# Kernel optimization log

Measured on AMD Instinct MI355X. Metric: run time of the kernel, lower is better.

Reference implementation:

```python
import jax, jax.numpy as jnp
import numpy as np

B = 1024
N_ATOMS = 51
FLAT = 7 * 7 * 64  # conv output: 84->20->9->7 spatial, 64 channels


def _conv(x, w, b, s):
    # x: NCHW, w: OIHW, VALID padding, stride s
    y = jax.lax.conv_general_dilated(
        x, w, window_strides=(s, s), padding='VALID',
        dimension_numbers=('NCHW', 'OIHW', 'NCHW'))
    return y + b[None, :, None, None]


def setup_inputs() -> dict:
    key = jax.random.key(0)
    ks = jax.random.split(key, 8)

    def w(k, shape, fan_in):
        return jax.random.normal(k, shape, dtype=jnp.float32) / np.float32(np.sqrt(fan_in))

    return {
        'x': jax.random.uniform(ks[0], (B, 4, 84, 84), jnp.float32, 0.0, 256.0),
        'cw1': w(ks[1], (32, 4, 8, 8), 4 * 8 * 8), 'cb1': jnp.zeros((32,), jnp.float32),
        'cw2': w(ks[2], (64, 32, 4, 4), 32 * 4 * 4), 'cb2': jnp.zeros((64,), jnp.float32),
        'cw3': w(ks[3], (64, 64, 3, 3), 64 * 3 * 3), 'cb3': jnp.zeros((64,), jnp.float32),
        'fw1': w(ks[4], (FLAT, 256), FLAT), 'fb1': jnp.zeros((256,), jnp.float32),
        'fw2': w(ks[5], (256, N_ATOMS), 256), 'fb2': jnp.zeros((N_ATOMS,), jnp.float32),
        'z': jnp.linspace(-10.0, 10.0, N_ATOMS).astype(jnp.float32),  # support atoms
        'n_out': 6,
    }


def reference(x, cw1, cb1, cw2, cb2, cw3, cb3, fw1, fb1, fw2, fb2, z, n_out):
    x = x / 256.0
    x = jax.nn.relu(_conv(x, cw1, cb1, 4))  # [B,32,20,20]
    x = jax.nn.relu(_conv(x, cw2, cb2, 2))  # [B,64,9,9]
    x = jax.nn.relu(_conv(x, cw3, cb3, 1))  # [B,64,7,7]
    h = x.reshape(x.shape[0], -1)           # [B,3136]
    h = jax.nn.relu(h @ fw1 + fb1)          # [B,256]
    p = jax.nn.softmax(h @ fw2 + fb2, axis=1)  # [B,n_atoms]
    # Original loop writes fc_layers(x)[i] identically for every action j:
    dist = jnp.broadcast_to(p[:, None, :], (p.shape[0], n_out, p.shape[1]))
    res = jnp.einsum('bna,a->bn', dist, z)  # expected value per action
    return (dist, res)
```

## Files before the change

kernel.cpp:

```cpp
#include <hip/hip_runtime.h>
#include <hip/hip_fp16.h>

#define RL(x) __builtin_amdgcn_readfirstlane(x)

typedef _Float16 f16x8 __attribute__((ext_vector_type(8)));
typedef float    f32x16 __attribute__((ext_vector_type(16)));

__global__ __launch_bounds__(256) void wprep_k(const float* __restrict__ w1,
                                               const float* __restrict__ w2,
                                               const float* __restrict__ w3,
                                               __half* __restrict__ w1h,
                                               __half* __restrict__ w2h,
                                               float* __restrict__ wt3) {
  int i = blockIdx.x * 256 + threadIdx.x;
  if (i < 8192) {
    int kx = i & 7, oc = (i >> 3) & 31, ky = (i >> 8) & 7, ic = i >> 11;
    w1h[i] = __float2half(w1[oc * 256 + ic * 64 + ky * 8 + kx] * 0.00390625f);
  }
  if (i < 32768) {
    int j = i & 7, ln = (i >> 3) & 31, kh = (i >> 8) & 1, ot = (i >> 9) & 1, ic = i >> 10;
    int k = kh * 8 + j, kx = k >> 2, ky = k & 3, oc = ot * 32 + ln;
    w2h[i] = __float2half(w2[oc * 512 + ic * 16 + ky * 4 + kx]);
  }
  if (i < 36864) {
    int o3 = i % 24, o = o3 / 3, kx = o3 - o * 3;
    int r = i / 24, ocg = r & 7, r2 = r >> 3, ky = r2 % 3, ic = r2 / 3;
    wt3[i] = w3[(ocg * 8 + o) * 576 + ic * 9 + ky * 3 + kx];
  }
}

__global__ __launch_bounds__(256, 2) void conv1_k(const float* __restrict__ x,
                                                  const __half* __restrict__ w1h,
                                                  const float* __restrict__ bias,
                                                  __half* __restrict__ out) {
  const int b = blockIdx.x;
  const int tid = threadIdx.x;
  const int lane = tid & 63;
  const int wv   = RL(tid >> 6);
  const int kh = lane >> 5;
  const int ln = lane & 31;
  const int nt = (wv == 0) ? 4 : 3;

  int ibs[4], pvv[4];
#pragma unroll
  for (int tt = 0; tt < 4; ++tt) {
    int p = (wv + tt * 4) * 32 + ln;
    pvv[tt] = (p < 400);
    if (p > 399) p = 399;
    int py = p / 20, px = p - py * 20;
    ibs[tt] = py * 336 + px * 4;
  }

  f32x16 acc[4];
#pragma unroll
  for (int tt = 0; tt < 4; ++tt)
#pragma unroll
    for (int r = 0; r < 16; ++r) acc[tt][r] = 0.f;

  const float* xb = x + b * 28224;

#pragma unroll 1
  for (int ic = 0; ic < 4; ++ic) {
#pragma unroll
    for (int t = 0; t < 4; ++t) {
      f16x8 aw = *(const f16x8*)(w1h + ((ic * 8 + 2 * t + kh) * 32 + ln) * 8);
      const float* rp = xb + ic * 7056 + (2 * t + kh) * 84;
#pragma unroll
      for (int tt = 0; tt < 4; ++tt) {
        if (tt < nt) {
          const float* ap = rp + ibs[tt];
          float4 lo = *(const float4*)ap;
          float4 hi = *(const float4*)(ap + 4);
          __half2 p0 = __floats2half2_rn(lo.x, lo.y);
          __half2 p1 = __floats2half2_rn(lo.z, lo.w);
          __half2 p2 = __floats2half2_rn(hi.x, hi.y);
          __half2 p3 = __floats2half2_rn(hi.z, hi.w);
          uint4 u = make_uint4(*(unsigned*)&p0, *(unsigned*)&p1,
                               *(unsigned*)&p2, *(unsigned*)&p3);
          f16x8 bx = *(f16x8*)&u;
          acc[tt] = __builtin_amdgcn_mfma_f32_32x32x16_f16(aw, bx, acc[tt], 0, 0, 0);
        }
      }
    }
  }

  float bv[16];
#pragma unroll
  for (int r = 0; r < 16; ++r)
    bv[r] = bias[(r & 3) + 8 * (r >> 2) + 4 * kh];

#pragma unroll
  for (int tt = 0; tt < 4; ++tt) {
    if (tt < nt && pvv[tt]) {
      const int p = (wv + tt * 4) * 32 + ln;
#pragma unroll
      for (int r = 0; r < 16; ++r) {
        const int oc = (r & 3) + 8 * (r >> 2) + 4 * kh;
        float v = acc[tt][r] + bv[r];
        out[b * 12800 + oc * 400 + p] = __float2half(v > 0.f ? v : 0.f);
      }
    }
  }
}

__global__ __launch_bounds__(256) void t1_k(const __half* __restrict__ in,
                                            __half* __restrict__ out) {
  __shared__ __half t[64][65];
  const int kb = blockIdx.x * 64;
  const int bb = blockIdx.y * 64;
  const int lane = threadIdx.x & 63;
  const int ty   = threadIdx.x >> 6;
#pragma unroll
  for (int r = ty; r < 64; r += 4)
    t[r][lane] = in[(bb + r) * 12800 + kb + lane];
  __syncthreads();
#pragma unroll
  for (int r = ty; r < 64; r += 4)
    out[(kb + r) * 1024 + bb + lane] = t[lane][r];
}

__global__ __launch_bounds__(256, 1) void conv2_k(const __half* __restrict__ in,
                                                  const __half* __restrict__ w2h,
                                                  const float* __restrict__ bias,
                                                  __half* __restrict__ out) {
  __shared__ __align__(16) __half sh[2][9216];
  const int bid = blockIdx.x;
  const int opy = bid % 9;
  const int bt  = bid / 9;
  const int bbase = bt * 64;
  const int tid  = threadIdx.x;
  const int lane = tid & 63;
  const int wv   = RL(tid >> 6);
  const int octile = wv & 1;
  const int bsub   = wv >> 1;
  const int kh = lane >> 5;
  const int ln = lane & 31;

  const unsigned short* inu = (const unsigned short*)in;
  const unsigned short* wu  = (const unsigned short*)w2h;

  int roff[5], offA[5];
#pragma unroll
  for (int p = 0; p < 5; ++p) {
    int idx = p * 256 + tid;
    int px = idx >> 6, b = idx & 63;
    roff[p] = px * 1024 + b;
    offA[p] = b * 128 + ((((px >> 1) ^ (b & 7)) << 3) | ((px & 1) << 2));
  }
  const int base0 = (40 * opy) * 1024 + bbase;

  f32x16 acc[9];
#pragma unroll
  for (int ox = 0; ox < 9; ++ox)
#pragma unroll
    for (int r = 0; r < 16; ++r) acc[ox][r] = 0.f;

  ushort4 s0, s1, s2, s3, s4; uint2 sW;

#define C2_LOAD(icv) do {                                                     \
    const unsigned short* ibp = inu + (icv) * 409600 + base0;                 \
    s0 = make_ushort4(ibp[roff[0]], ibp[roff[0]+20480], ibp[roff[0]+40960], ibp[roff[0]+61440]); \
    s1 = make_ushort4(ibp[roff[1]], ibp[roff[1]+20480], ibp[roff[1]+40960], ibp[roff[1]+61440]); \
    s2 = make_ushort4(ibp[roff[2]], ibp[roff[2]+20480], ibp[roff[2]+40960], ibp[roff[2]+61440]); \
    s3 = make_ushort4(ibp[roff[3]], ibp[roff[3]+20480], ibp[roff[3]+40960], ibp[roff[3]+61440]); \
    s4 = make_ushort4(ibp[roff[4]], ibp[roff[4]+20480], ibp[roff[4]+40960], ibp[roff[4]+61440]); \
    sW = *(const uint2*)(wu + (icv) * 1024 + tid * 4);                        \
  } while (0)

#define C2_STORE(buf) do {                                                    \
    *(uint2*)&sh[buf][offA[0]] = make_uint2((unsigned)s0.x | ((unsigned)s0.y << 16), (unsigned)s0.z | ((unsigned)s0.w << 16)); \
    *(uint2*)&sh[buf][offA[1]] = make_uint2((unsigned)s1.x | ((unsigned)s1.y << 16), (unsigned)s1.z | ((unsigned)s1.w << 16)); \
    *(uint2*)&sh[buf][offA[2]] = make_uint2((unsigned)s2.x | ((unsigned)s2.y << 16), (unsigned)s2.z | ((unsigned)s2.w << 16)); \
    *(uint2*)&sh[buf][offA[3]] = make_uint2((unsigned)s3.x | ((unsigned)s3.y << 16), (unsigned)s3.z | ((unsigned)s3.w << 16)); \
    *(uint2*)&sh[buf][offA[4]] = make_uint2((unsigned)s4.x | ((unsigned)s4.y << 16), (unsigned)s4.z | ((unsigned)s4.w << 16)); \
    *(uint2*)&sh[buf][8192 + tid * 4] = sW;                                   \
  } while (0)

  const int offW = 8192 + octile * 512 + kh * 256 + ln * 8;
  const int bloc = bsub * 32 + ln;
  const int bx7  = bloc & 7;
  const int brow = bloc * 128;

  int cur = 0;
  C2_LOAD(0);
#pragma unroll 1
  for (int ic = 0; ic < 32; ++ic) {
    __syncthreads();
    C2_STORE(cur);
    const int icn = ic < 31 ? ic + 1 : 31;
    C2_LOAD(icn);
    __syncthreads();
    f16x8 aw = *(const f16x8*)&sh[cur][offW];
#pragma unroll
    for (int ox = 0; ox < 9; ++ox) {
      f16x8 bx = *(const f16x8*)&sh[cur][brow + (((ox + kh) ^ bx7) << 3)];
      acc[ox] = __builtin_amdgcn_mfma_f32_32x32x16_f16(aw, bx, acc[ox], 0, 0, 0);
    }
    cur ^= 1;
  }
#undef C2_LOAD
#undef C2_STORE

  float bv[16];
#pragma unroll
  for (int r = 0; r < 16; ++r)
    bv[r] = bias[octile * 32 + (r & 3) + 8 * (r >> 2) + 4 * kh];
  const int bout = bbase + bloc;
#pragma unroll
  for (int ox = 0; ox < 9; ++ox) {
#pragma unroll
    for (int r = 0; r < 16; ++r) {
      const int oc = octile * 32 + (r & 3) + 8 * (r >> 2) + 4 * kh;
      float v = acc[ox][r] + bv[r];
      out[(oc * 81 + opy * 9 + ox) * 1024 + bout] = __float2half(v > 0.f ? v : 0.f);
    }
  }
}

__global__ __launch_bounds__(128, 2) void conv3_k(const __half* __restrict__ in,
                                                  const float* __restrict__ wt,
                                                  const float* __restrict__ bias,
                                                  __half* __restrict__ out) {
  const int bid = blockIdx.x;
  const int ocg = (bid >> 3) & 15;
  const int grp = ((bid >> 7) << 3) | (bid & 7);
  const int opy = grp % 7;
  const int bg  = grp / 7;
  const int tid  = threadIdx.x;
  const int lane = tid & 63;
  const int wv   = RL(tid >> 6);

  float acc[4][7];
#pragma unroll
  for (int o = 0; o < 4; ++o)
#pragma unroll
    for (int ox = 0; ox < 7; ++ox) acc[o][ox] = 0.f;

  const __half* ib = in + bg * 64 + lane;
  const int ic0 = wv * 32;

#pragma unroll 1
  for (int ici = 0; ici < 32; ++ici) {
    const int ic = ic0 + ici;
#pragma unroll
    for (int ky = 0; ky < 3; ++ky) {
      const float* wp = wt + ((ic * 3 + ky) * 8 + (ocg >> 1)) * 24 + (ocg & 1) * 12;
      float wk[12];
#pragma unroll
      for (int q = 0; q < 12; ++q) wk[q] = wp[q];
      const __half* rp = ib + (ic * 81 + (opy + ky) * 9) * 1024;
      float iv[9];
#pragma unroll
      for (int q = 0; q < 9; ++q) iv[q] = __half2float(rp[q * 1024]);
#pragma unroll
      for (int o = 0; o < 4; ++o)
#pragma unroll
        for (int ox = 0; ox < 7; ++ox)
#pragma unroll
          for (int kx = 0; kx < 3; ++kx)
            acc[o][ox] = fmaf(iv[ox + kx], wk[o * 3 + kx], acc[o][ox]);
    }
  }

  __shared__ float red[4][7][64];
  if (wv == 1) {
#pragma unroll
    for (int o = 0; o < 4; ++o)
#pragma unroll
      for (int ox = 0; ox < 7; ++ox) red[o][ox][lane] = acc[o][ox];
  }
  __syncthreads();
  if (wv == 0) {
#pragma unroll
    for (int o = 0; o < 4; ++o) {
      const int oc = ocg * 4 + o;
      const float bj = bias[oc];
#pragma unroll
      for (int ox = 0; ox < 7; ++ox) {
        float v = acc[o][ox] + red[o][ox][lane] + bj;
        out[(oc * 49 + opy * 7 + ox) * 1024 + bg * 64 + lane] =
            __float2half(v > 0.f ? v : 0.f);
      }
    }
  }
}

__global__ __launch_bounds__(64, 2) void fc1a_k(const __half* __restrict__ a,
                                                const float* __restrict__ w,
                                                float* __restrict__ part) {
  const int bid = blockIdx.x;
  const int jg  = (bid >> 3) & 15;
  const int grp = ((bid >> 7) << 3) | (bid & 7);
  const int kc  = grp & 15;
  const int bg  = grp >> 4;
  const int lane = threadIdx.x;

  float acc[16];
#pragma unroll
  for (int j = 0; j < 16; ++j) acc[j] = 0.f;

  const __half* ap = a + kc * 196 * 1024 + bg * 64 + lane;
  const float* wp0 = w + kc * 196 * 256 + jg * 16;

#pragma unroll 4
  for (int k = 0; k < 196; ++k) {
    float av = __half2float(ap[k * 1024]);
    const float* wp = wp0 + k * 256;
#pragma unroll
    for (int j = 0; j < 16; ++j) acc[j] = fmaf(av, wp[j], acc[j]);
  }
#pragma unroll
  for (int j = 0; j < 16; ++j)
    part[(kc * 256 + jg * 16 + j) * 1024 + bg * 64 + lane] = acc[j];
}

__global__ __launch_bounds__(256) void fc1b_k(const float* __restrict__ part,
                                              const float* __restrict__ bias,
                                              float* __restrict__ h) {
  int idx = blockIdx.x * 256 + threadIdx.x;
  float s = bias[idx >> 10];
#pragma unroll
  for (int c = 0; c < 16; ++c) s += part[c * 262144 + idx];
  h[idx] = s > 0.f ? s : 0.f;
}

__global__ __launch_bounds__(256) void fc2_k(const float* __restrict__ h,
                                             const float* __restrict__ w,
                                             const float* __restrict__ bias,
                                             const float* __restrict__ z,
                                             float* __restrict__ dist,
                                             float* __restrict__ res) {
  __shared__ float wl[256 * 51];
  const int tid = threadIdx.x;
#pragma unroll
  for (int i = tid; i < 256 * 51; i += 256) wl[i] = w[i];
  __syncthreads();

  const int j   = tid & 63;
  const int b   = blockIdx.x * 4 + RL(tid >> 6);
  const int jc = j < 51 ? j : 50;
  float acc = bias[jc];
#pragma unroll 8
  for (int k = 0; k < 256; ++k)
    acc = fmaf(h[k * 1024 + b], wl[k * 51 + jc], acc);
  float logit = (j < 51) ? acc : -1e30f;
  float m = logit;
#pragma unroll
  for (int o = 32; o > 0; o >>= 1) m = fmaxf(m, __shfl_xor(m, o, 64));
  float e = (j < 51) ? __expf(logit - m) : 0.f;
  float ssum = e;
#pragma unroll
  for (int o = 32; o > 0; o >>= 1) ssum += __shfl_xor(ssum, o, 64);
  float p = e / ssum;
  float zv = (j < 51) ? z[jc] : 0.f;
  float rz = p * zv;
#pragma unroll
  for (int o = 32; o > 0; o >>= 1) rz += __shfl_xor(rz, o, 64);
  if (j < 51) {
    float* db = dist + b * 6 * 51 + j;
#pragma unroll
    for (int n = 0; n < 6; ++n) db[n * 51] = p;
  }
  if (j < 6) res[b * 6 + j] = rz;
}

extern "C" void kernel_launch(void* const* d_in, const int* in_sizes, int n_in,
                              void* d_out, int out_size, void* d_ws, size_t ws_size,
                              hipStream_t stream) {
  const float* x   = (const float*)d_in[0];
  const float* cw1 = (const float*)d_in[1];
  const float* cb1 = (const float*)d_in[2];
  const float* cw2 = (const float*)d_in[3];
  const float* cb2 = (const float*)d_in[4];
  const float* cw3 = (const float*)d_in[5];
  const float* cb3 = (const float*)d_in[6];
  const float* fw1 = (const float*)d_in[7];
  const float* fb1 = (const float*)d_in[8];
  const float* fw2 = (const float*)d_in[9];
  const float* fb2 = (const float*)d_in[10];
  const float* z   = (const float*)d_in[11];

  float* ws = (float*)d_ws;
  __half* c1h = (__half*)ws;
  __half* c1t = (__half*)(ws + 6553600);
  __half* c2t = (__half*)(ws + 13107200);
  __half* c3t = (__half*)(ws + 15761408);
  float*  pw  = ws;
  float*  h_t = ws + 4194304;

  float*  wt3n = (float*)d_out;
  __half* w1h  = (__half*)((float*)d_out + 36864);
  __half* w2h  = (__half*)((float*)d_out + 45056);

  float* dist = (float*)d_out;
  float* res  = dist + 1024 * 6 * 51;

  wprep_k<<<144, 256, 0, stream>>>(cw1, cw2, cw3, w1h, w2h, wt3n);
  conv1_k<<<1024, 256, 0, stream>>>(x, w1h, cb1, c1h);
  t1_k<<<dim3(200, 16), 256, 0, stream>>>(c1h, c1t);
  conv2_k<<<144, 256, 0, stream>>>(c1t, w2h, cb2, c2t);
  conv3_k<<<1792, 128, 0, stream>>>(c2t, wt3n, cb3, c3t);
  fc1a_k<<<4096, 64, 0, stream>>>(c3t, fw1, pw);
  fc1b_k<<<1024, 256, 0, stream>>>(pw, fb1, h_t);
  fc2_k<<<256, 256, 0, stream>>>(h_t, fw2, fb2, z, dist, res);
}
```

Baseline: 395.4 us.

## Rewrite conv3 as f16 MFMA with double-buffered LDS staging

```diff
diff --git a/kernel.cpp b/kernel.cpp
--- a/kernel.cpp
+++ b/kernel.cpp
@@ -4,6 +4,7 @@
 #define RL(x) __builtin_amdgcn_readfirstlane(x)
 
 typedef _Float16 f16x8 __attribute__((ext_vector_type(8)));
+typedef _Float16 f16x4 __attribute__((ext_vector_type(4)));
 typedef float    f32x16 __attribute__((ext_vector_type(16)));
 
 __global__ __launch_bounds__(256) void wprep_k(const float* __restrict__ w1,
@@ -11,7 +12,7 @@
                                                const float* __restrict__ w3,
                                                __half* __restrict__ w1h,
                                                __half* __restrict__ w2h,
-                                               float* __restrict__ wt3) {
+                                               __half* __restrict__ w3h) {
   int i = blockIdx.x * 256 + threadIdx.x;
   if (i < 8192) {
     int kx = i & 7, oc = (i >> 3) & 31, ky = (i >> 8) & 7, ic = i >> 11;
@@ -22,10 +23,11 @@
     int k = kh * 8 + j, kx = k >> 2, ky = k & 3, oc = ot * 32 + ln;
     w2h[i] = __float2half(w2[oc * 512 + ic * 16 + ky * 4 + kx]);
   }
-  if (i < 36864) {
-    int o3 = i % 24, o = o3 / 3, kx = o3 - o * 3;
-    int r = i / 24, ocg = r & 7, r2 = r >> 3, ky = r2 % 3, ic = r2 / 3;
-    wt3[i] = w3[(ocg * 8 + o) * 576 + ic * 9 + ky * 3 + kx];
+  if (i < 65536) {
+    int j = i & 7, ln = (i >> 3) & 31, kh = (i >> 8) & 1, ot = (i >> 9) & 1, ic = i >> 10;
+    int k = kh * 8 + j, kx = k >> 2, ky = k & 3, oc = ot * 32 + ln;
+    float v = (kx < 3 && ky < 3) ? w3[oc * 576 + ic * 9 + ky * 3 + kx] : 0.f;
+    w3h[i] = __float2half(v);
   }
 }
 
@@ -217,70 +219,111 @@
   }
 }
 
-__global__ __launch_bounds__(128, 2) void conv3_k(const __half* __restrict__ in,
-                                                  const float* __restrict__ wt,
+__global__ __launch_bounds__(256, 1) void conv3_k(const __half* __restrict__ in,
+                                                  const __half* __restrict__ w3h,
                                                   const float* __restrict__ bias,
                                                   __half* __restrict__ out) {
+  __shared__ __align__(16) __half sh[2][3840];
   const int bid = blockIdx.x;
-  const int ocg = (bid >> 3) & 15;
-  const int grp = ((bid >> 7) << 3) | (bid & 7);
-  const int opy = grp % 7;
-  const int bg  = grp / 7;
+  const int opy = bid % 7;
+  const int bt  = bid / 7;
+  const int bbase = bt * 64;
   const int tid  = threadIdx.x;
   const int lane = tid & 63;
   const int wv   = RL(tid >> 6);
-
-  float acc[4][7];
-#pragma unroll
-  for (int o = 0; o < 4; ++o)
-#pragma unroll
-    for (int ox = 0; ox < 7; ++ox) acc[o][ox] = 0.f;
-
-  const __half* ib = in + bg * 64 + lane;
-  const int ic0 = wv * 32;
-
+  const int octile = wv & 1;
+  const int bsub   = wv >> 1;
+  const int kh = lane >> 5;
+  const int ln = lane & 31;
+
+  const unsigned short* inu = (const unsigned short*)in;
+  const unsigned short* wu  = (const unsigned short*)w3h;
+
+  int rof[4];
+#pragma unroll
+  for (int ky = 0; ky < 4; ++ky) {
+    int r = opy + ky; if (r > 8) r = 8;
+    rof[ky] = r * 9 * 1024;
+  }
+  int gof[3], sof[3];
+#pragma unroll
+  for (int p = 0; p < 3; ++p) {
+    int idx = p * 256 + tid;
+    int b = idx & 63, px = idx >> 6;
+    int pxc = px > 8 ? 8 : px;
+    gof[p] = pxc * 1024 + bbase + b;
+    sof[p] = b * 44 + px * 4;
+  }
+
+  f32x16 acc[7];
+#pragma unroll
+  for (int ox = 0; ox < 7; ++ox)
+#pragma unroll
+    for (int r = 0; r < 16; ++r) acc[ox][r] = 0.f;
+
+  ushort4 s0, s1, s2; uint2 sW;
+
+#define C3_LOAD(icv) do {                                                     \
+    const unsigned short* ibp = inu + (icv) * 82944;                          \
+    s0 = make_ushort4(ibp[rof[0]+gof[0]], ibp[rof[1]+gof[0]],                 \
+                      ibp[rof[2]+gof[0]], ibp[rof[3]+gof[0]]);                \
+    s1 = make_ushort4(ibp[rof[0]+gof[1]], ibp[rof[1]+gof[1]],                 \
+                      ibp[rof[2]+gof[1]], ibp[rof[3]+gof[1]]);                \
+    if (tid < 128)                                                            \
+      s2 = make_ushort4(ibp[rof[0]+gof[2]], ibp[rof[1]+gof[2]],               \
+                        ibp[rof[2]+gof[2]], ibp[rof[3]+gof[2]]);              \
+    sW = *(const uint2*)(wu + (icv) * 1024 + tid * 4);                        \
+  } while (0)
+
+#define C3_STORE(buf) do {                                                    \
+    *(uint2*)&sh[buf][sof[0]] = make_uint2((unsigned)s0.x | ((unsigned)s0.y << 16), (unsigned)s0.z | ((unsigned)s0.w << 16)); \
+    *(uint2*)&sh[buf][sof[1]] = make_uint2((unsigned)s1.x | ((unsigned)s1.y << 16), (unsigned)s1.z | ((unsigned)s1.w << 16)); \
+    if (tid < 128)                                                            \
+      *(uint2*)&sh[buf][sof[2]] = make_uint2((unsigned)s2.x | ((unsigned)s2.y << 16), (unsigned)s2.z | ((unsigned)s2.w << 16)); \
+    *(uint2*)&sh[buf][2816 + tid * 4] = sW;                                   \
+  } while (0)
+
+  const int offW = 2816 + octile * 512 + kh * 256 + ln * 8;
+  const int bloc = bsub * 32 + ln;
+  const int brow = bloc * 44;
+
+  int cur = 0;
+  C3_LOAD(0);
 #pragma unroll 1
-  for (int ici = 0; ici < 32; ++ici) {
-    const int ic = ic0 + ici;
-#pragma unroll
-    for (int ky = 0; ky < 3; ++ky) {
-      const float* wp = wt + ((ic * 3 + ky) * 8 + (ocg >> 1)) * 24 + (ocg & 1) * 12;
-      float wk[12];
-#pragma unroll
-      for (int q = 0; q < 12; ++q) wk[q] = wp[q];
-      const __half* rp = ib + (ic * 81 + (opy + ky) * 9) * 1024;
-      float iv[9];
-#pragma unroll
-      for (int q = 0; q < 9; ++q) iv[q] = __half2float(rp[q * 1024]);
-#pragma unroll
-      for (int o = 0; o < 4; ++o)
-#pragma unroll
-        for (int ox = 0; ox < 7; ++ox)
-#pragma unroll
-          for (int kx = 0; kx < 3; ++kx)
-            acc[o][ox] = fmaf(iv[ox + kx], wk[o * 3 + kx], acc[o][ox]);
-    }
-  }
-
-  __shared__ float red[4][7][64];
-  if (wv == 1) {
-#pragma unroll
-    for (int o = 0; o < 4; ++o)
-#pragma unroll
-      for (int ox = 0; ox < 7; ++ox) red[o][ox][lane] = acc[o][ox];
-  }
-  __syncthreads();
-  if (wv == 0) {
-#pragma unroll
-    for (int o = 0; o < 4; ++o) {
-      const int oc = ocg * 4 + o;
-      const float bj = bias[oc];
-#pragma unroll
-      for (int ox = 0; ox < 7; ++ox) {
-        float v = acc[o][ox] + red[o][ox][lane] + bj;
-        out[(oc * 49 + opy * 7 + ox) * 1024 + bg * 64 + lane] =
-            __float2half(v > 0.f ? v : 0.f);
-      }
+  for (int ic = 0; ic < 64; ++ic) {
+    __syncthreads();
+    C3_STORE(cur);
+    const int icn = ic < 63 ? ic + 1 : 63;
+    C3_LOAD(icn);
+    __syncthreads();
+    f16x8 aw = *(const f16x8*)&sh[cur][offW];
+#pragma unroll
+    for (int ox = 0; ox < 7; ++ox) {
+      const int p0 = ox + 2 * kh;
+      f16x4 lo = *(const f16x4*)&sh[cur][brow + p0 * 4];
+      f16x4 hi = *(const f16x4*)&sh[cur][brow + p0 * 4 + 4];
+      f16x8 bx;
+      bx[0]=lo[0]; bx[1]=lo[1]; bx[2]=lo[2]; bx[3]=lo[3];
+      bx[4]=hi[0]; bx[5]=hi[1]; bx[6]=hi[2]; bx[7]=hi[3];
+      acc[ox] = __builtin_amdgcn_mfma_f32_32x32x16_f16(aw, bx, acc[ox], 0, 0, 0);
+    }
+    cur ^= 1;
+  }
+#undef C3_LOAD
+#undef C3_STORE
+
+  float bv[16];
+#pragma unroll
+  for (int r = 0; r < 16; ++r)
+    bv[r] = bias[octile * 32 + (r & 3) + 8 * (r >> 2) + 4 * kh];
+  const int bout = bbase + bloc;
+#pragma unroll
+  for (int ox = 0; ox < 7; ++ox) {
+#pragma unroll
+    for (int r = 0; r < 16; ++r) {
+      const int oc = octile * 32 + (r & 3) + 8 * (r >> 2) + 4 * kh;
+      float v = acc[ox][r] + bv[r];
+      out[(oc * 49 + opy * 7 + ox) * 1024 + bout] = __float2half(v > 0.f ? v : 0.f);
     }
   }
 }
@@ -388,18 +431,18 @@
   float*  pw  = ws;
   float*  h_t = ws + 4194304;
 
-  float*  wt3n = (float*)d_out;
+  __half* w3h  = (__half*)d_out;
   __half* w1h  = (__half*)((float*)d_out + 36864);
   __half* w2h  = (__half*)((float*)d_out + 45056);
 
   float* dist = (float*)d_out;
   float* res  = dist + 1024 * 6 * 51;
 
-  wprep_k<<<144, 256, 0, stream>>>(cw1, cw2, cw3, w1h, w2h, wt3n);
+  wprep_k<<<256, 256, 0, stream>>>(cw1, cw2, cw3, w1h, w2h, w3h);
   conv1_k<<<1024, 256, 0, stream>>>(x, w1h, cb1, c1h);
   t1_k<<<dim3(200, 16), 256, 0, stream>>>(c1h, c1t);
   conv2_k<<<144, 256, 0, stream>>>(c1t, w2h, cb2, c2t);
-  conv3_k<<<1792, 128, 0, stream>>>(c2t, wt3n, cb3, c3t);
+  conv3_k<<<112, 256, 0, stream>>>(c2t, w3h, cb3, c3t);
   fc1a_k<<<4096, 64, 0, stream>>>(c3t, fw1, pw);
   fc1b_k<<<1024, 256, 0, stream>>>(pw, fb1, h_t);
   fc2_k<<<256, 256, 0, stream>>>(h_t, fw2, fb2, z, dist, res);
```

Measured after the change: 366.1 us. -7.4%, faster.
